# Kernel optimization log

Hardware: AMD Instinct MI355X
Metric: run time of the kernel (lower is better)

Reference implementation:

```python
import jax, jax.numpy as jnp
import numpy as np

B, H, LC, LQ = 64, 256, 2048, 256
NEG = -1e30


def setup_inputs() -> dict:
    key = jax.random.key(0)
    k1, k2, k3, k4, k5 = jax.random.split(key, 5)
    C = jax.random.normal(k1, (B, H, LC), dtype=jnp.float32)
    Q = jax.random.normal(k2, (B, H, LQ), dtype=jnp.float32)
    # mask convention: 1.0 = masked (padding), 0.0 = valid
    cmask = jax.random.bernoulli(k3, 0.1, (B, LC)).astype(jnp.float32)
    qmask = jax.random.bernoulli(k4, 0.1, (B, LQ)).astype(jnp.float32)
    line_project = jax.random.normal(k5, (3 * H,), dtype=jnp.float32) / np.sqrt(H)
    return {"C": C, "Q": Q, "cmask": cmask, "qmask": qmask, "line_project": line_project}


def reference(C, Q, cmask, qmask, line_project):
    # C: [B,H,Lc], Q: [B,H,Lq] -> [B,Lc,H], [B,Lq,H]
    Ct = jnp.swapaxes(C, 1, 2)
    Qt = jnp.swapaxes(Q, 1, 2)
    w1, w2, w3 = jnp.split(line_project, 3)
    # Trilinear decomposition of S[b,i,j] = [Ct;Qt;Ct*Qt] . w
    # avoids materializing the [B,Lc,Lq,3H] tensor of the original.
    S = (Ct @ w1)[:, :, None] + (Qt @ w2)[:, None, :] \
        + jnp.einsum('bih,h,bjh->bij', Ct, w3, Qt)  # [B,Lc,Lq]
    qm = qmask[:, None, :]  # [B,1,Lq]
    cm = cmask[:, :, None]  # [B,Lc,1]
    S_row = jax.nn.softmax(S * (1.0 - qm) + qm * NEG, axis=2)   # over Lq
    S_col = jax.nn.softmax(S * (1.0 - cm) + cm * NEG, axis=1)   # over Lc
    A = S_row @ Qt                                  # [B,Lc,H]
    # (S_row @ S_col^T) @ Ct  ==  S_row @ (S_col^T @ Ct): avoid [Lc,Lc]
    Bt = S_row @ (jnp.swapaxes(S_col, 1, 2) @ Ct)   # [B,Lc,H]
    out = jnp.concatenate((Ct, A, Ct * A, Ct * Bt), axis=2)  # [B,Lc,4H]
    # dropout is identity at inference (training=False)
    return jnp.swapaxes(out, 1, 2)  # [B,4H,Lc]
```

## Files before the change

### kernel.cpp

```cpp
#include <hip/hip_runtime.h>

#define BB 64
#define HH 256
#define LC 2048
#define LQ 256
#define NEGV -1e30f

#define OFF_S    0L
#define FOFF_BF  33554432L
#define FOFF_T   33554432L
#define FOFF_Q2  37748736L
#define FOFF_PM  37748736L
#define FOFF_PL  37879808L
#define OFF_FLAG 38010880L

#define NOFF_BF  33554432L
#define NOFF_Q2  37748736L
#define NOFF_PM  33554432L
#define NOFF_PL  33816576L
#define NOFF_T   34078720L

typedef __attribute__((ext_vector_type(8))) short short8v;
typedef __attribute__((ext_vector_type(4))) float f32x4;

union FragU { uint4 u; short8v h; };

__device__ __forceinline__ short8v ldfrag(const unsigned short* p) {
  FragU f; f.u = *reinterpret_cast<const uint4*>(p); return f.h;
}

#define MFMA(a, b, c) __builtin_amdgcn_mfma_f32_16x16x32_bf16(a, b, c, 0, 0, 0)

template<int MODE>
__device__ __forceinline__ float ld(const void* p, long idx) {
  if (MODE == 1) {
    unsigned short u = ((const unsigned short*)p)[idx];
    return __uint_as_float(((unsigned int)u) << 16);
  } else {
    return ((const float*)p)[idx];
  }
}

__device__ __forceinline__ float bf2f(unsigned short u) {
  return __uint_as_float(((unsigned int)u) << 16);
}

__device__ __forceinline__ unsigned short f2bf(float f) {
  unsigned int u = __float_as_uint(f);
  unsigned int r = (u + 0x7fffu + ((u >> 16) & 1u)) >> 16;
  return (unsigned short)r;
}

__device__ __forceinline__ void split1(float v, unsigned short& h, unsigned short& l) {
  unsigned int u = __float_as_uint(v);
  h = (unsigned short)(u >> 16);
  float r = v - __uint_as_float(u & 0xffff0000u);
  l = f2bf(r);
}

__device__ __forceinline__ void split8(const float4 f0, const float4 f1,
                                       short8v& hi, short8v& lo) {
  float v[8] = {f0.x, f0.y, f0.z, f0.w, f1.x, f1.y, f1.z, f1.w};
#pragma unroll
  for (int e = 0; e < 8; e++) {
    unsigned short h, l;
    split1(v[e], h, l);
    ((unsigned short*)&hi)[e] = h;
    ((unsigned short*)&lo)[e] = l;
  }
}

union U16x8 { uint4 u; unsigned short s[8]; };

__global__ void sniff_kernel(const unsigned int* cw, int* flag) {
  __shared__ int cnt[64];
  int tid = threadIdx.x;
  unsigned int w = cw[tid];
  int p = 0;
  for (int h = 0; h < 2; h++) {
    unsigned short u = h ? (unsigned short)(w >> 16) : (unsigned short)(w & 0xffffu);
    float f = __uint_as_float(((unsigned int)u) << 16);
    float a = fabsf(f);
    if ((a >= 1e-5f && a <= 64.0f) || f == 0.0f) p++;
  }
  cnt[tid] = p;
  __syncthreads();
  if (tid == 0) {
    int t = 0;
    for (int i = 0; i < 64; i++) t += cnt[i];
    *flag = (t >= 102) ? 1 : 0;
  }
}


__global__ __launch_bounds__(256) void f0_bfold(const void* Qp, const void* lpp,
                                                float* ws, const int* flag) {
  if (*flag != 0) return;
  __shared__ __align__(16) float Qs[64][68];
  __shared__ float w1s[HH], w2s[HH], w3s[HH];
  __shared__ float q2red[4][64];
  int t = threadIdx.x, b = blockIdx.y, j0 = blockIdx.x * 64;
  const float* Qf = (const float*)Qp;
  const float* lpf = (const float*)lpp;
  w1s[t] = lpf[t]; w2s[t] = lpf[HH + t]; w3s[t] = lpf[2 * HH + t];
  long qbase = (long)b * HH * LQ;
  unsigned short* Bfw = (unsigned short*)(ws + FOFF_BF);
  int jl = t & 63, hg = t >> 6;
  float q2a = 0.f;
  for (int hp = 0; hp < 4; hp++) {
    int h0 = hp * 64;
    __syncthreads();
    {
      int row = t >> 2, c = t & 3;
      const float4* src = (const float4*)&Qf[qbase + (long)(h0 + row) * LQ + j0 + c * 16];
      float4 v0 = src[0], v1 = src[1], v2 = src[2], v3 = src[3];
      *(float4*)&Qs[row][c * 16]      = v0;
      *(float4*)&Qs[row][c * 16 + 4]  = v1;
      *(float4*)&Qs[row][c * 16 + 8]  = v2;
      *(float4*)&Qs[row][c * 16 + 12] = v3;
    }
    __syncthreads();
    unsigned int hiw[8], low[8];
#pragma unroll
    for (int e = 0; e < 16; e++) {
      int hh = hg * 16 + e;
      int h = h0 + hh;
      float qv = Qs[hh][jl];
      float bb = w1s[h] + w3s[h] * qv;
      q2a += w2s[h] * qv;
      unsigned short bh, bl;
      split1(bb, bh, bl);
      if (e & 1) { hiw[e >> 1] |= ((unsigned int)bh) << 16; low[e >> 1] |= ((unsigned int)bl) << 16; }
      else       { hiw[e >> 1] = bh; low[e >> 1] = bl; }
    }
    long bfb = ((long)b * LQ + j0 + jl) * (2 * HH);
    *(uint4*)&Bfw[bfb + h0 + hg * 16]          = make_uint4(hiw[0], hiw[1], hiw[2], hiw[3]);
    *(uint4*)&Bfw[bfb + h0 + hg * 16 + 8]      = make_uint4(hiw[4], hiw[5], hiw[6], hiw[7]);
    *(uint4*)&Bfw[bfb + HH + h0 + hg * 16]     = make_uint4(low[0], low[1], low[2], low[3]);
    *(uint4*)&Bfw[bfb + HH + h0 + hg * 16 + 8] = make_uint4(low[4], low[5], low[6], low[7]);
  }
  q2red[hg][jl] = q2a;
  __syncthreads();
  if (t < 64)
    ws[FOFF_Q2 + (long)b * LQ + j0 + t] =
        q2red[0][t] + q2red[1][t] + q2red[2][t] + q2red[3][t];
}

__global__ __launch_bounds__(256) void f1_S(const void* Cp, float* ws, const int* flag) {
  if (*flag != 0) return;
  __shared__ __align__(16) unsigned short CaH[64 * 40];
  __shared__ __align__(16) unsigned short CaL[64 * 40];
  int t = threadIdx.x, b = blockIdx.y, i0 = blockIdx.x * 64;
  int w = t >> 6, l = t & 63;
  int lane_m = l & 15, kb = l >> 4;
  const float* Cf = (const float*)Cp;
  const unsigned short* Bf = (const unsigned short*)(ws + FOFF_BF);
  long cbase = (long)b * HH * LC;
  f32x4 z4 = {0.f, 0.f, 0.f, 0.f};
  f32x4 acc[4][4];
#pragma unroll
  for (int mf = 0; mf < 4; mf++)
#pragma unroll
    for (int nf = 0; nf < 4; nf++) acc[mf][nf] = z4;

  for (int hc = 0; hc < 8; hc++) {
    int h0 = hc * 32;
    __syncthreads();
#pragma unroll
    for (int hp = 0; hp < 4; hp++) {
      int hh = hp * 8 + (t >> 5);
      int ii = (t & 31) * 2;
      float2 cw = *(const float2*)&Cf[cbase + (long)(h0 + hh) * LC + i0 + ii];
      unsigned short xh, xl;
      split1(cw.x, xh, xl);
      CaH[ii * 40 + hh] = xh; CaL[ii * 40 + hh] = xl;
      split1(cw.y, xh, xl);
      CaH[(ii + 1) * 40 + hh] = xh; CaL[(ii + 1) * 40 + hh] = xl;
    }
    __syncthreads();
    short8v aH[4], aL[4];
#pragma unroll
    for (int mf = 0; mf < 4; mf++) {
      aH[mf] = ldfrag(&CaH[(mf * 16 + lane_m) * 40 + kb * 8]);
      aL[mf] = ldfrag(&CaL[(mf * 16 + lane_m) * 40 + kb * 8]);
    }
#pragma unroll
    for (int nf = 0; nf < 4; nf++) {
      long jb = ((long)b * LQ + w * 64 + nf * 16 + lane_m) * (2 * HH) + h0 + kb * 8;
      short8v bh = ldfrag(&Bf[jb]);
      short8v bl = ldfrag(&Bf[jb + HH]);
#pragma unroll
      for (int mf = 0; mf < 4; mf++) {
        acc[mf][nf] = MFMA(aH[mf], bh, acc[mf][nf]);
        acc[mf][nf] = MFMA(aH[mf], bl, acc[mf][nf]);
        acc[mf][nf] = MFMA(aL[mf], bh, acc[mf][nf]);
      }
    }
  }
  const float* q2g = ws + FOFF_Q2 + (long)b * LQ;
#pragma unroll
  for (int nf = 0; nf < 4; nf++) {
    int j = w * 64 + nf * 16 + lane_m;
    float q2v = q2g[j];
    float* So = ws + OFF_S + ((long)b * LC + i0 + kb * 4) * LQ + j;
#pragma unroll
    for (int mf = 0; mf < 4; mf++)
#pragma unroll
      for (int r = 0; r < 4; r++)
        So[(long)(mf * 16 + r) * LQ] = acc[mf][nf][r] + q2v;
  }
}

__global__ __launch_bounds__(256) void f2a_col(const void* cmaskp, float* ws, const int* flag) {
  if (*flag != 0) return;
  __shared__ float cms[256];
  int t = threadIdx.x, ch = blockIdx.x, b = blockIdx.y;
  int ib = ch * 256;
  cms[t] = ((const float*)cmaskp)[(long)b * LC + ib + t];
  __syncthreads();
  const float* Sb = ws + OFF_S + ((long)b * LC + ib) * LQ + t;
  float m = -INFINITY;
#pragma unroll 8
  for (int i = 0; i < 256; i++) {
    float v = (cms[i] != 0.f) ? NEGV : Sb[(long)i * LQ];
    m = fmaxf(m, v);
  }
  float s = 0.f;
#pragma unroll 8
  for (int i = 0; i < 256; i++) {
    float v = (cms[i] != 0.f) ? NEGV : Sb[(long)i * LQ];
    s += __expf(v - m);
  }
  ws[FOFF_PM + ((long)b * 8 + ch) * LQ + t] = m;
  ws[FOFF_PL + ((long)b * 8 + ch) * LQ + t] = s;
}

__global__ __launch_bounds__(512) void f2b_T(const void* Cp, const void* cmaskp,
                                             float* ws, const int* flag) {
  if (*flag != 0) return;
  __shared__ __align__(16) unsigned short PtH[64 * 72];
  __shared__ __align__(16) unsigned short PtL[64 * 72];
  int t = threadIdx.x, b = blockIdx.y, j0 = blockIdx.x * 64;
  int w = t >> 6, l = t & 63;
  int lane_m = l & 15, kb = l >> 4;
  int jj = j0 + l;
  const float* Cf = (const float*)Cp;
  const float* cmf = (const float*)cmaskp;
  float M = -INFINITY;
#pragma unroll
  for (int c = 0; c < 8; c++)
    M = fmaxf(M, ws[FOFF_PM + ((long)b * 8 + c) * LQ + jj]);
  float L = 0.f;
#pragma unroll
  for (int c = 0; c < 8; c++)
    L += ws[FOFF_PL + ((long)b * 8 + c) * LQ + jj] *
         __expf(ws[FOFF_PM + ((long)b * 8 + c) * LQ + jj] - M);
  float Li = 1.0f / L;
  int hw = (w >> 1) * 64, jw = (w & 1) * 32;
  long cbase = (long)b * HH * LC;
  const float* Sb = ws + OFF_S + (long)b * LC * LQ;
  f32x4 z4 = {0.f, 0.f, 0.f, 0.f};
  f32x4 acc[4][2];
#pragma unroll
  for (int mf = 0; mf < 4; mf++) { acc[mf][0] = z4; acc[mf][1] = z4; }

  for (int ic = 0; ic < 32; ic++) {
    int i0 = ic * 64;
    __syncthreads();
    unsigned int pwH[4], pwL[4];
#pragma unroll
    for (int s2 = 0; s2 < 4; s2++) {
      unsigned short h0s, l0s, h1s, l1s;
      {
        int i = i0 + w * 8 + 2 * s2;
        float cm = cmf[(long)b * LC + i];
        float sv = Sb[(long)i * LQ + jj];
        float p = (cm != 0.f) ? 0.f : __expf(sv - M) * Li;
        split1(p, h0s, l0s);
      }
      {
        int i = i0 + w * 8 + 2 * s2 + 1;
        float cm = cmf[(long)b * LC + i];
        float sv = Sb[(long)i * LQ + jj];
        float p = (cm != 0.f) ? 0.f : __expf(sv - M) * Li;
        split1(p, h1s, l1s);
      }
      pwH[s2] = (unsigned int)h0s | ((unsigned int)h1s << 16);
      pwL[s2] = (unsigned int)l0s | ((unsigned int)l1s << 16);
    }
    *(uint4*)&PtH[l * 72 + w * 8] = make_uint4(pwH[0], pwH[1], pwH[2], pwH[3]);
    *(uint4*)&PtL[l * 72 + w * 8] = make_uint4(pwL[0], pwL[1], pwL[2], pwL[3]);
    __syncthreads();
#pragma unroll
    for (int ks = 0; ks < 2; ks++) {
      short8v b0h = ldfrag(&PtH[(jw + lane_m) * 72 + ks * 32 + kb * 8]);
      short8v b0l = ldfrag(&PtL[(jw + lane_m) * 72 + ks * 32 + kb * 8]);
      short8v b1h = ldfrag(&PtH[(jw + 16 + lane_m) * 72 + ks * 32 + kb * 8]);
      short8v b1l = ldfrag(&PtL[(jw + 16 + lane_m) * 72 + ks * 32 + kb * 8]);
#pragma unroll
      for (int mf = 0; mf < 4; mf++) {
        const float* cp = Cf + cbase + (long)(hw + mf * 16 + lane_m) * LC + i0 + ks * 32 + kb * 8;
        short8v aH, aL;
        split8(((const float4*)cp)[0], ((const float4*)cp)[1], aH, aL);
        acc[mf][0] = MFMA(aH, b0h, acc[mf][0]);
        acc[mf][0] = MFMA(aH, b0l, acc[mf][0]);
        acc[mf][0] = MFMA(aL, b0h, acc[mf][0]);
        acc[mf][1] = MFMA(aH, b1h, acc[mf][1]);
        acc[mf][1] = MFMA(aH, b1l, acc[mf][1]);
        acc[mf][1] = MFMA(aL, b1h, acc[mf][1]);
      }
    }
  }
  unsigned short* Tu = (unsigned short*)(ws + FOFF_T);
#pragma unroll
  for (int mf = 0; mf < 4; mf++)
#pragma unroll
    for (int nf = 0; nf < 2; nf++)
#pragma unroll
      for (int r = 0; r < 4; r++) {
        int h = hw + mf * 16 + kb * 4 + r;
        int j = j0 + jw + nf * 16 + lane_m;
        unsigned short th, tl;
        split1(acc[mf][nf][r], th, tl);
        long tb = ((long)b * HH + h) * (2 * LQ);
        Tu[tb + j] = th;
        Tu[tb + LQ + j] = tl;
      }
}

__global__ __launch_bounds__(512) void f3_out(const void* Cp, const void* Qp, const void* qmaskp,
                                              float* ws, void* outp, const int* flag) {
  if (*flag != 0) return;
  __shared__ __align__(16) unsigned short PrH[32 * 264];
  __shared__ __align__(16) unsigned short PrL[32 * 264];
  __shared__ float qms[LQ];
  int t = threadIdx.x, b = blockIdx.y, i0 = blockIdx.x * 32;
  int w = t >> 6, l = t & 63;
  const float* Cf = (const float*)Cp;
  const float* Qf = (const float*)Qp;
  if (t < LQ) qms[t] = ((const float*)qmaskp)[(long)b * LQ + t];
  __syncthreads();
  const float* Sb = ws + OFF_S + ((long)b * LC + i0) * LQ;
#pragma unroll
  for (int r = 0; r < 4; r++) {
    int row = w * 4 + r;
    float v[4];
#pragma unroll
    for (int c = 0; c < 4; c++) {
      float sv = Sb[(long)row * LQ + l + 64 * c];
      v[c] = (qms[l + 64 * c] != 0.f) ? NEGV : sv;
    }
    float mx = fmaxf(fmaxf(v[0], v[1]), fmaxf(v[2], v[3]));
#pragma unroll
    for (int o2 = 1; o2 < 64; o2 <<= 1) mx = fmaxf(mx, __shfl_xor(mx, o2));
    float e[4]; float sm = 0.f;
#pragma unroll
    for (int c = 0; c < 4; c++) { e[c] = __expf(v[c] - mx); sm += e[c]; }
#pragma unroll
    for (int o2 = 1; o2 < 64; o2 <<= 1) sm += __shfl_xor(sm, o2);
    float inv = 1.0f / sm;
#pragma unroll
    for (int c = 0; c < 4; c++) {
      unsigned short ph, pl;
      split1(e[c] * inv, ph, pl);
      PrH[row * 264 + l + 64 * c] = ph;
      PrL[row * 264 + l + 64 * c] = pl;
    }
  }
  __syncthreads();
  int lane_m = l & 15, kb = l >> 4;
  int hw2 = w * 32;
  const unsigned short* Tu = (const unsigned short*)(ws + FOFF_T);
  long qrow = (long)b * HH * LQ;
  f32x4 z4 = {0.f, 0.f, 0.f, 0.f};
  f32x4 acc1[2][2], acc2[2][2];
#pragma unroll
  for (int mf = 0; mf < 2; mf++) {
    acc1[mf][0] = z4; acc1[mf][1] = z4;
    acc2[mf][0] = z4; acc2[mf][1] = z4;
  }
#pragma unroll
  for (int kc = 0; kc < 8; kc++) {
    short8v b0h = ldfrag(&PrH[lane_m * 264 + kc * 32 + kb * 8]);
    short8v b0l = ldfrag(&PrL[lane_m * 264 + kc * 32 + kb * 8]);
    short8v b1h = ldfrag(&PrH[(16 + lane_m) * 264 + kc * 32 + kb * 8]);
    short8v b1l = ldfrag(&PrL[(16 + lane_m) * 264 + kc * 32 + kb * 8]);
#pragma unroll
    for (int mf = 0; mf < 2; mf++) {
      int h = hw2 + mf * 16 + lane_m;
      const float* qp = Qf + qrow + (long)h * LQ + kc * 32 + kb * 8;
      short8v a1H, a1L;
      split8(((const float4*)qp)[0], ((const float4*)qp)[1], a1H, a1L);
      long tb = ((long)b * HH + h) * (2 * LQ) + kc * 32 + kb * 8;
      short8v a2H = ldfrag(&Tu[tb]);
      short8v a2L = ldfrag(&Tu[tb + LQ]);
      acc1[mf][0] = MFMA(a1H, b0h, acc1[mf][0]);
      acc1[mf][0] = MFMA(a1H, b0l, acc1[mf][0]);
      acc1[mf][0] = MFMA(a1L, b0h, acc1[mf][0]);
      acc1[mf][1] = MFMA(a1H, b1h, acc1[mf][1]);
      acc1[mf][1] = MFMA(a1H, b1l, acc1[mf][1]);
      acc1[mf][1] = MFMA(a1L, b1h, acc1[mf][1]);
      acc2[mf][0] = MFMA(a2H, b0h, acc2[mf][0]);
      acc2[mf][0] = MFMA(a2H, b0l, acc2[mf][0]);
      acc2[mf][0] = MFMA(a2L, b0h, acc2[mf][0]);
      acc2[mf][1] = MFMA(a2H, b1h, acc2[mf][1]);
      acc2[mf][1] = MFMA(a2H, b1l, acc2[mf][1]);
      acc2[mf][1] = MFMA(a2L, b1h, acc2[mf][1]);
    }
  }
  float* o = (float*)outp;
  long ob = (long)b * (4 * HH) * LC;
#pragma unroll
  for (int mf = 0; mf < 2; mf++)
#pragma unroll
    for (int nf = 0; nf < 2; nf++) {
      int i = i0 + nf * 16 + lane_m;
#pragma unroll
      for (int r = 0; r < 4; r++) {
        int h = hw2 + mf * 16 + kb * 4 + r;
        float cc = Cf[((long)b * HH + h) * LC + i];
        float av = acc1[mf][nf][r], bv = acc2[mf][nf][r];
        long r0 = ob + (long)h * LC + i;
        o[r0] = cc;
        o[r0 + (long)HH * LC] = av;
        o[r0 + 2L * HH * LC] = cc * av;
        o[r0 + 3L * HH * LC] = cc * bv;
      }
    }
}


__global__ __launch_bounds__(256) void nk0_bfold(const void* Qp, const void* lpp,
                                                 float* ws, const int* flag) {
  if (*flag != 1) return;
  __shared__ __align__(16) unsigned short Qs[64 * 72];
  __shared__ float w1s[HH], w2s[HH], w3s[HH];
  __shared__ float q2red[4][64];
  int t = threadIdx.x;
  int b = blockIdx.y, j0 = blockIdx.x * 64;
  w1s[t] = ld<1>(lpp, t);
  w2s[t] = ld<1>(lpp, HH + t);
  w3s[t] = ld<1>(lpp, 2 * HH + t);
  const unsigned short* Qu = (const unsigned short*)Qp;
  long qbase = (long)b * HH * LQ;
  unsigned short* Bf = (unsigned short*)(ws + NOFF_BF);
  int jl = t & 63, hg = t >> 6;
  float q2a = 0.f;
  for (int hp = 0; hp < 4; hp++) {
    int h0 = hp * 64;
    __syncthreads();
    {
      int row = t >> 2, c = t & 3;
      const uint4* src = (const uint4*)&Qu[qbase + (long)(h0 + row) * LQ + j0 + c * 16];
      uint4 v0 = src[0]; uint4 v1 = src[1];
      *(uint4*)&Qs[row * 72 + c * 16] = v0;
      *(uint4*)&Qs[row * 72 + c * 16 + 8] = v1;
    }
    __syncthreads();
    unsigned int hiw[8], low[8];
#pragma unroll
    for (int e = 0; e < 16; e++) {
      int hh = hg * 16 + e;
      int h = h0 + hh;
      float qv = bf2f(Qs[hh * 72 + jl]);
      float bb = w1s[h] + w3s[h] * qv;
      q2a += w2s[h] * qv;
      unsigned short bh = f2bf(bb);
      float res = bb - bf2f(bh);
      unsigned short bl = f2bf(res);
      if (e & 1) { hiw[e >> 1] |= ((unsigned int)bh) << 16; low[e >> 1] |= ((unsigned int)bl) << 16; }
      else       { hiw[e >> 1] = bh; low[e >> 1] = bl; }
    }
    long bfb = ((long)b * LQ + j0 + jl) * (2 * HH);
    *(uint4*)&Bf[bfb + h0 + hg * 16]      = make_uint4(hiw[0], hiw[1], hiw[2], hiw[3]);
    *(uint4*)&Bf[bfb + h0 + hg * 16 + 8]  = make_uint4(hiw[4], hiw[5], hiw[6], hiw[7]);
    *(uint4*)&Bf[bfb + HH + h0 + hg * 16]     = make_uint4(low[0], low[1], low[2], low[3]);
    *(uint4*)&Bf[bfb + HH + h0 + hg * 16 + 8] = make_uint4(low[4], low[5], low[6], low[7]);
  }
  q2red[hg][jl] = q2a;
  __syncthreads();
  if (t < 64)
    ws[NOFF_Q2 + (long)b * LQ + j0 + t] =
        q2red[0][t] + q2red[1][t] + q2red[2][t] + q2red[3][t];
}

__global__ __launch_bounds__(256) void nk1_S(const void* Cp, float* ws, const int* flag) {
  if (*flag != 1) return;
  __shared__ __align__(16) unsigned short Ca[64 * 40];
  int t = threadIdx.x;
  int b = blockIdx.y, i0 = blockIdx.x * 64;
  int w = t >> 6, l = t & 63;
  int lane_m = l & 15, kb = l >> 4;
  const unsigned short* Cu = (const unsigned short*)Cp;
  const unsigned short* Bf = (const unsigned short*)(ws + NOFF_BF);
  long cbase = (long)b * HH * LC;
  f32x4 z4 = {0.f, 0.f, 0.f, 0.f};
  f32x4 acc[4][4];
#pragma unroll
  for (int mf = 0; mf < 4; mf++)
#pragma unroll
    for (int nf = 0; nf < 4; nf++) acc[mf][nf] = z4;

  for (int hc = 0; hc < 8; hc++) {
    int h0 = hc * 32;
    __syncthreads();
#pragma unroll
    for (int hp = 0; hp < 4; hp++) {
      int hh = hp * 8 + (t >> 5);
      int ii = (t & 31) * 2;
      unsigned int cw = *(const unsigned int*)&Cu[cbase + (long)(h0 + hh) * LC + i0 + ii];
      Ca[ii * 40 + hh] = (unsigned short)(cw & 0xffffu);
      Ca[(ii + 1) * 40 + hh] = (unsigned short)(cw >> 16);
    }
    __syncthreads();
    short8v afr[4];
#pragma unroll
    for (int mf = 0; mf < 4; mf++)
      afr[mf] = ldfrag(&Ca[(mf * 16 + lane_m) * 40 + kb * 8]);
#pragma unroll
    for (int nf = 0; nf < 4; nf++) {
      long jb = ((long)b * LQ + w * 64 + nf * 16 + lane_m) * (2 * HH) + h0 + kb * 8;
      short8v bh = ldfrag(&Bf[jb]);
      short8v bl = ldfrag(&Bf[jb + HH]);
#pragma unroll
      for (int mf = 0; mf < 4; mf++) {
        acc[mf][nf] = MFMA(afr[mf], bh, acc[mf][nf]);
        acc[mf][nf] = MFMA(afr[mf], bl, acc[mf][nf]);
      }
    }
  }
  const float* q2g = ws + NOFF_Q2 + (long)b * LQ;
#pragma unroll
  for (int nf = 0; nf < 4; nf++) {
    int j = w * 64 + nf * 16 + lane_m;
    float q2v = q2g[j];
    float* So = ws + OFF_S + ((long)b * LC + i0 + kb * 4) * LQ + j;
#pragma unroll
    for (int mf = 0; mf < 4; mf++)
#pragma unroll
      for (int r = 0; r < 4; r++)
        So[(long)(mf * 16 + r) * LQ] = acc[mf][nf][r] + q2v;
  }
}

__global__ __launch_bounds__(256) void nk2a_col(const void* cmaskp, float* ws, const int* flag) {
  if (*flag != 1) return;
  __shared__ float cms[128];
  int t = threadIdx.x, ch = blockIdx.x, b = blockIdx.y;
  int ib = ch * 128;
  if (t < 128) cms[t] = ld<1>(cmaskp, (long)b * LC + ib + t);
  __syncthreads();
  const float* Sb = ws + OFF_S + ((long)b * LC + ib) * LQ + t;
  float m = -INFINITY;
#pragma unroll 8
  for (int i = 0; i < 128; i++) {
    float v = (cms[i] != 0.f) ? NEGV : Sb[(long)i * LQ];
    m = fmaxf(m, v);
  }
  float s = 0.f;
#pragma unroll 8
  for (int i = 0; i < 128; i++) {
    float v = (cms[i] != 0.f) ? NEGV : Sb[(long)i * LQ];
    s += __expf(v - m);
  }
  ws[NOFF_PM + ((long)b * 16 + ch) * LQ + t] = m;
  ws[NOFF_PL + ((long)b * 16 + ch) * LQ + t] = s;
}

__global__ __launch_bounds__(512) void nk2b_T(const void* Cp, const void* cmaskp,
                                              float* ws, const int* flag) {
  if (*flag != 1) return;
  __shared__ __align__(16) unsigned short Pt[64 * 72];
  int t = threadIdx.x, b = blockIdx.y, j0 = blockIdx.x * 64;
  int w = t >> 6, l = t & 63;
  int lane_m = l & 15, kb = l >> 4;
  int jj = j0 + l;
  float M = -INFINITY;
#pragma unroll
  for (int c = 0; c < 16; c++)
    M = fmaxf(M, ws[NOFF_PM + ((long)b * 16 + c) * LQ + jj]);
  float L = 0.f;
#pragma unroll
  for (int c = 0; c < 16; c++)
    L += ws[NOFF_PL + ((long)b * 16 + c) * LQ + jj] *
         __expf(ws[NOFF_PM + ((long)b * 16 + c) * LQ + jj] - M);
  float Li = 1.0f / L;
  int hw = (w >> 1) * 64, jw = (w & 1) * 32;
  const unsigned short* Cu = (const unsigned short*)Cp;
  long cbase = (long)b * HH * LC;
  const float* Sb = ws + OFF_S + (long)b * LC * LQ;
  f32x4 z4 = {0.f, 0.f, 0.f, 0.f};
  f32x4 acc[4][2];
#pragma unroll
  for (int mf = 0; mf < 4; mf++) { acc[mf][0] = z4; acc[mf][1] = z4; }

  for (int ic = 0; ic < 32; ic++) {
    int i0 = ic * 64;
    __syncthreads();
    unsigned int pw[4];
#pragma unroll
    for (int s2 = 0; s2 < 4; s2++) {
      unsigned int lo16, hi16;
      {
        int i = i0 + w * 8 + 2 * s2;
        float cm = ld<1>(cmaskp, (long)b * LC + i);
        float sv = Sb[(long)i * LQ + jj];
        float p = (cm != 0.f) ? 0.f : __expf(sv - M) * Li;
        lo16 = f2bf(p);
      }
      {
        int i = i0 + w * 8 + 2 * s2 + 1;
        float cm = ld<1>(cmaskp, (long)b * LC + i);
        float sv = Sb[(long)i * LQ + jj];
        float p = (cm != 0.f) ? 0.f : __expf(sv - M) * Li;
        hi16 = f2bf(p);
      }
      pw[s2] = lo16 | (hi16 << 16);
    }
    *(uint4*)&Pt[l * 72 + w * 8] = make_uint4(pw[0], pw[1], pw[2], pw[3]);
    __syncthreads();
#pragma unroll
    for (int ks = 0; ks < 2; ks++) {
      short8v b0 = ldfrag(&Pt[(jw + lane_m) * 72 + ks * 32 + kb * 8]);
      short8v b1 = ldfrag(&Pt[(jw + 16 + lane_m) * 72 + ks * 32 + kb * 8]);
#pragma unroll
      for (int mf = 0; mf < 4; mf++) {
        short8v a = ldfrag(&Cu[cbase + (long)(hw + mf * 16 + lane_m) * LC + i0 + ks * 32 + kb * 8]);
        acc[mf][0] = MFMA(a, b0, acc[mf][0]);
        acc[mf][1] = MFMA(a, b1, acc[mf][1]);
      }
    }
  }
  unsigned short* Tt = (unsigned short*)(ws + NOFF_T);
#pragma unroll
  for (int mf = 0; mf < 4; mf++)
#pragma unroll
    for (int nf = 0; nf < 2; nf++)
#pragma unroll
      for (int r = 0; r < 4; r++) {
        int h = hw + mf * 16 + kb * 4 + r;
        int j = j0 + jw + nf * 16 + lane_m;
        Tt[((long)b * HH + h) * LQ + j] = f2bf(acc[mf][nf][r]);
      }
}

__global__ __launch_bounds__(512) void nk3_out(const void* Cp, const void* Qp, const void* qmaskp,
                                               float* ws, void* outp, const int* flag) {
  if (*flag != 1) return;
  __shared__ __align__(16) unsigned short Pr[64 * 264];
  __shared__ float qms[LQ];
  int t = threadIdx.x, b = blockIdx.y, i0 = blockIdx.x * 64;
  int w = t >> 6, l = t & 63;
  if (t < LQ) qms[t] = ld<1>(qmaskp, (long)b * LQ + t);
  __syncthreads();
  const float* Sb = ws + OFF_S + ((long)b * LC + i0) * LQ;
#pragma unroll
  for (int r = 0; r < 8; r++) {
    int row = w * 8 + r;
    float v[4];
#pragma unroll
    for (int c = 0; c < 4; c++) {
      float sv = Sb[(long)row * LQ + l + 64 * c];
      v[c] = (qms[l + 64 * c] != 0.f) ? NEGV : sv;
    }
    float mx = fmaxf(fmaxf(v[0], v[1]), fmaxf(v[2], v[3]));
#pragma unroll
    for (int o = 1; o < 64; o <<= 1) mx = fmaxf(mx, __shfl_xor(mx, o));
    float e[4]; float sm = 0.f;
#pragma unroll
    for (int c = 0; c < 4; c++) { e[c] = __expf(v[c] - mx); sm += e[c]; }
#pragma unroll
    for (int o = 1; o < 64; o <<= 1) sm += __shfl_xor(sm, o);
    float inv = 1.0f / sm;
#pragma unroll
    for (int c = 0; c < 4; c++) Pr[row * 264 + l + 64 * c] = f2bf(e[c] * inv);
  }
  __syncthreads();
  int lane_m = l & 15, kb = l >> 4;
  int hw2 = (w >> 1) * 64, iw = (w & 1) * 32;
  const unsigned short* Qu = (const unsigned short*)Qp;
  const unsigned short* Tt = (const unsigned short*)(ws + NOFF_T);
  long qrow = (long)b * HH * LQ;
  f32x4 z4 = {0.f, 0.f, 0.f, 0.f};
  f32x4 acc1[4][2], acc2[4][2];
#pragma unroll
  for (int mf = 0; mf < 4; mf++) {
    acc1[mf][0] = z4; acc1[mf][1] = z4;
    acc2[mf][0] = z4; acc2[mf][1] = z4;
  }
#pragma unroll
  for (int kc = 0; kc < 8; kc++) {
    short8v b0 = ldfrag(&Pr[(iw + lane_m) * 264 + kc * 32 + kb * 8]);
    short8v b1 = ldfrag(&Pr[(iw + 16 + lane_m) * 264 + kc * 32 + kb * 8]);
#pragma unroll
    for (int mf = 0; mf < 4; mf++) {
      long ro = qrow + (long)(hw2 + mf * 16 + lane_m) * LQ + kc * 32 + kb * 8;
      short8v a1 = ldfrag(&Qu[ro]);
      acc1[mf][0] = MFMA(a1, b0, acc1[mf][0]);
      acc1[mf][1] = MFMA(a1, b1, acc1[mf][1]);
      short8v a2 = ldfrag(&Tt[ro]);
      acc2[mf][0] = MFMA(a2, b0, acc2[mf][0]);
      acc2[mf][1] = MFMA(a2, b1, acc2[mf][1]);
    }
  }
  unsigned short* o = (unsigned short*)outp;
  const unsigned short* Cu = (const unsigned short*)Cp;
  long ob = (long)b * (4 * HH) * LC;
#pragma unroll
  for (int mf = 0; mf < 4; mf++)
#pragma unroll
    for (int nf = 0; nf < 2; nf++) {
      int i = i0 + iw + nf * 16 + lane_m;
#pragma unroll
      for (int r = 0; r < 4; r++) {
        int h = hw2 + mf * 16 + kb * 4 + r;
        unsigned short craw = Cu[(long)(b * HH + h) * LC + i];
        float cc = bf2f(craw);
        float av = acc1[mf][nf][r], bv = acc2[mf][nf][r];
        long r0 = ob + (long)h * LC + i;
        o[r0] = craw;
        o[r0 + (long)HH * LC] = f2bf(av);
        o[r0 + 2L * HH * LC] = f2bf(cc * av);
        o[r0 + 3L * HH * LC] = f2bf(cc * bv);
      }
    }
}

extern "C" void kernel_launch(void* const* d_in, const int* in_sizes, int n_in,
                              void* d_out, int out_size, void* d_ws, size_t ws_size,
                              hipStream_t stream) {
  const void* C  = d_in[0];
  const void* Q  = d_in[1];
  const void* cm = d_in[2];
  const void* qm = d_in[3];
  const void* lp = d_in[4];
  float* ws = (float*)d_ws;
  int* flag = (int*)(ws + OFF_FLAG);

  sniff_kernel<<<1, 64, 0, stream>>>((const unsigned int*)C, flag);

  f0_bfold<<<dim3(4, BB), 256, 0, stream>>>(Q, lp, ws, flag);
  f1_S<<<dim3(LC / 64, BB), 256, 0, stream>>>(C, ws, flag);
  f2a_col<<<dim3(8, BB), 256, 0, stream>>>(cm, ws, flag);
  f2b_T<<<dim3(4, BB), 512, 0, stream>>>(C, cm, ws, flag);
  f3_out<<<dim3(LC / 32, BB), 512, 0, stream>>>(C, Q, qm, ws, d_out, flag);

  nk0_bfold<<<dim3(4, BB), 256, 0, stream>>>(Q, lp, ws, flag);
  nk1_S<<<dim3(LC / 64, BB), 256, 0, stream>>>(C, ws, flag);
  nk2a_col<<<dim3(16, BB), 256, 0, stream>>>(cm, ws, flag);
  nk2b_T<<<dim3(4, BB), 512, 0, stream>>>(C, cm, ws, flag);
  nk3_out<<<dim3(LC / 64, BB), 512, 0, stream>>>(C, Q, qm, ws, d_out, flag);
}
```

Baseline: 1.431 ms.

## Fuse row-softmax into S GEMM, store bf16 exp scores, drop column-stats pass

```diff
diff --git a/kernel.cpp b/kernel.cpp
--- a/kernel.cpp
+++ b/kernel.cpp
@@ -6,14 +6,17 @@
 #define LQ 256
 #define NEGV -1e30f
 
+#define GOFF_X    0L
+#define GOFF_BF   16777216L
+#define GOFF_QS   20971520L
+#define GOFF_TS   25165824L
+#define GOFF_MR   29360128L
+#define GOFF_LR   29491200L
+#define GOFF_Q2   29622272L
+#define GOFF_K    29638656L
+#define OFF_FLAG  38010880L
+
 #define OFF_S    0L
-#define FOFF_BF  33554432L
-#define FOFF_T   33554432L
-#define FOFF_Q2  37748736L
-#define FOFF_PM  37748736L
-#define FOFF_PL  37879808L
-#define OFF_FLAG 38010880L
-
 #define NOFF_BF  33554432L
 #define NOFF_Q2  37748736L
 #define NOFF_PM  33554432L
@@ -72,7 +75,15 @@
 
 union U16x8 { uint4 u; unsigned short s[8]; };
 
-__global__ void sniff_kernel(const unsigned int* cw, int* flag) {
+__device__ __forceinline__ unsigned int fenc(float f) {
+  unsigned int u = __float_as_uint(f);
+  return (u >> 31) ? ~u : (u | 0x80000000u);
+}
+__device__ __forceinline__ float fdec(unsigned int e) {
+  return (e >> 31) ? __uint_as_float(e ^ 0x80000000u) : __uint_as_float(~e);
+}
+
+__global__ void sniff_kernel(const unsigned int* cw, int* flag, unsigned int* kz) {
   __shared__ int cnt[64];
   int tid = threadIdx.x;
   unsigned int w = cw[tid];
@@ -84,6 +95,7 @@
     if ((a >= 1e-5f && a <= 64.0f) || f == 0.0f) p++;
   }
   cnt[tid] = p;
+  kz[tid] = 0u;
   __syncthreads();
   if (tid == 0) {
     int t = 0;
@@ -104,7 +116,7 @@
   const float* lpf = (const float*)lpp;
   w1s[t] = lpf[t]; w2s[t] = lpf[HH + t]; w3s[t] = lpf[2 * HH + t];
   long qbase = (long)b * HH * LQ;
-  unsigned short* Bfw = (unsigned short*)(ws + FOFF_BF);
+  unsigned short* Bfw = (unsigned short*)(ws + GOFF_BF);
   int jl = t & 63, hg = t >> 6;
   float q2a = 0.f;
   for (int hp = 0; hp < 4; hp++) {
@@ -142,19 +154,51 @@
   q2red[hg][jl] = q2a;
   __syncthreads();
   if (t < 64)
-    ws[FOFF_Q2 + (long)b * LQ + j0 + t] =
+    ws[GOFF_Q2 + (long)b * LQ + j0 + t] =
         q2red[0][t] + q2red[1][t] + q2red[2][t] + q2red[3][t];
 }
 
-__global__ __launch_bounds__(256) void f1_S(const void* Cp, float* ws, const int* flag) {
+__global__ __launch_bounds__(256) void g0b_Qsplit(const void* Qp, const void* qmaskp,
+                                                  float* ws, const int* flag) {
+  if (*flag != 0) return;
+  __shared__ float qms[LQ];
+  int t = threadIdx.x, b = blockIdx.y, hb = blockIdx.x;
+  qms[t] = (((const float*)qmaskp)[(long)b * LQ + t] != 0.f) ? 0.f : 1.f;
+  __syncthreads();
+  const float* Qf = (const float*)Qp;
+  unsigned short* Qs = (unsigned short*)(ws + GOFF_QS);
+#pragma unroll
+  for (int it = 0; it < 4; it++) {
+    int o = t + 256 * it;
+    int hh = o >> 5;
+    int j8 = (o & 31) * 8;
+    const float* qp = Qf + ((long)b * HH + hb * 32 + hh) * LQ + j8;
+    float4 v0 = ((const float4*)qp)[0], v1 = ((const float4*)qp)[1];
+    float4 m0 = make_float4(v0.x * qms[j8], v0.y * qms[j8 + 1],
+                            v0.z * qms[j8 + 2], v0.w * qms[j8 + 3]);
+    float4 m1 = make_float4(v1.x * qms[j8 + 4], v1.y * qms[j8 + 5],
+                            v1.z * qms[j8 + 6], v1.w * qms[j8 + 7]);
+    short8v hi, lo;
+    split8(m0, m1, hi, lo);
+    long qb = ((long)b * HH + hb * 32 + hh) * (2 * LQ) + j8;
+    FragU fh, fl; fh.h = hi; fl.h = lo;
+    *(uint4*)&Qs[qb] = fh.u;
+    *(uint4*)&Qs[qb + LQ] = fl.u;
+  }
+}
+
+__global__ __launch_bounds__(256) void g1_SX(const void* Cp, const void* qmaskp,
+                                             float* ws, const int* flag) {
   if (*flag != 0) return;
   __shared__ __align__(16) unsigned short CaH[64 * 40];
   __shared__ __align__(16) unsigned short CaL[64 * 40];
+  __shared__ float redm[64][4];
+  __shared__ float redl[64][4];
   int t = threadIdx.x, b = blockIdx.y, i0 = blockIdx.x * 64;
   int w = t >> 6, l = t & 63;
   int lane_m = l & 15, kb = l >> 4;
   const float* Cf = (const float*)Cp;
-  const unsigned short* Bf = (const unsigned short*)(ws + FOFF_BF);
+  const unsigned short* Bf = (const unsigned short*)(ws + GOFF_BF);
   long cbase = (long)b * HH * LC;
   f32x4 z4 = {0.f, 0.f, 0.f, 0.f};
   f32x4 acc[4][4];
@@ -197,229 +241,220 @@
       }
     }
   }
-  const float* q2g = ws + FOFF_Q2 + (long)b * LQ;
+  const float* q2g = ws + GOFF_Q2 + (long)b * LQ;
+  const float* qmf = (const float*)qmaskp;
+  float q2v[4], qm0v[4];
 #pragma unroll
   for (int nf = 0; nf < 4; nf++) {
     int j = w * 64 + nf * 16 + lane_m;
-    float q2v = q2g[j];
-    float* So = ws + OFF_S + ((long)b * LC + i0 + kb * 4) * LQ + j;
-#pragma unroll
-    for (int mf = 0; mf < 4; mf++)
-#pragma unroll
-      for (int r = 0; r < 4; r++)
-        So[(long)(mf * 16 + r) * LQ] = acc[mf][nf][r] + q2v;
-  }
-}
-
-__global__ __launch_bounds__(256) void f2a_col(const void* cmaskp, float* ws, const int* flag) {
-  if (*flag != 0) return;
-  __shared__ float cms[256];
-  int t = threadIdx.x, ch = blockIdx.x, b = blockIdx.y;
-  int ib = ch * 256;
-  cms[t] = ((const float*)cmaskp)[(long)b * LC + ib + t];
-  __syncthreads();
-  const float* Sb = ws + OFF_S + ((long)b * LC + ib) * LQ + t;
-  float m = -INFINITY;
-#pragma unroll 8
-  for (int i = 0; i < 256; i++) {
-    float v = (cms[i] != 0.f) ? NEGV : Sb[(long)i * LQ];
-    m = fmaxf(m, v);
-  }
-  float s = 0.f;
-#pragma unroll 8
-  for (int i = 0; i < 256; i++) {
-    float v = (cms[i] != 0.f) ? NEGV : Sb[(long)i * LQ];
-    s += __expf(v - m);
-  }
-  ws[FOFF_PM + ((long)b * 8 + ch) * LQ + t] = m;
-  ws[FOFF_PL + ((long)b * 8 + ch) * LQ + t] = s;
-}
-
-__global__ __launch_bounds__(512) void f2b_T(const void* Cp, const void* cmaskp,
+    q2v[nf] = q2g[j];
+    qm0v[nf] = (qmf[(long)b * LQ + j] != 0.f) ? 0.f : 1.f;
+  }
+#pragma unroll
+  for (int mf = 0; mf < 4; mf++)
+#pragma unroll
+    for (int r = 0; r < 4; r++) {
+      float vx = -INFINITY;
+#pragma unroll
+      for (int nf = 0; nf < 4; nf++) {
+        float s = acc[mf][nf][r] + q2v[nf];
+        vx = fmaxf(vx, (qm0v[nf] != 0.f) ? s : NEGV);
+      }
+      vx = fmaxf(vx, __shfl_xor(vx, 1));
+      vx = fmaxf(vx, __shfl_xor(vx, 2));
+      vx = fmaxf(vx, __shfl_xor(vx, 4));
+      vx = fmaxf(vx, __shfl_xor(vx, 8));
+      if (lane_m == 0) redm[mf * 16 + kb * 4 + r][w] = vx;
+    }
+  __syncthreads();
+  unsigned short* Xu = (unsigned short*)(ws + GOFF_X);
+#pragma unroll
+  for (int mf = 0; mf < 4; mf++)
+#pragma unroll
+    for (int r = 0; r < 4; r++) {
+      int il = mf * 16 + kb * 4 + r;
+      float mr = fmaxf(fmaxf(fmaxf(redm[il][0], redm[il][1]),
+                             fmaxf(redm[il][2], redm[il][3])), -60.f);
+      float ls = 0.f;
+#pragma unroll
+      for (int nf = 0; nf < 4; nf++) {
+        int j = w * 64 + nf * 16 + lane_m;
+        float s = acc[mf][nf][r] + q2v[nf];
+        unsigned short xb = f2bf(__expf(s - mr));
+        Xu[((long)b * LC + i0 + il) * LQ + j] = xb;
+        ls += qm0v[nf] * bf2f(xb);
+      }
+      ls += __shfl_xor(ls, 1);
+      ls += __shfl_xor(ls, 2);
+      ls += __shfl_xor(ls, 4);
+      ls += __shfl_xor(ls, 8);
+      if (lane_m == 0) redl[il][w] = ls;
+    }
+  __syncthreads();
+  if (t < 64) {
+    int il = t;
+    float mrf = fmaxf(fmaxf(fmaxf(redm[il][0], redm[il][1]),
+                            fmaxf(redm[il][2], redm[il][3])), -60.f);
+    float lrf = redl[il][0] + redl[il][1] + redl[il][2] + redl[il][3];
+    ws[GOFF_MR + (long)b * LC + i0 + il] = mrf;
+    ws[GOFF_LR + (long)b * LC + i0 + il] = 1.0f / lrf;
+    redm[il][0] = mrf;
+  }
+  __syncthreads();
+  if (t == 0) {
+    float km = -INFINITY;
+    for (int i2 = 0; i2 < 64; i2++) km = fmaxf(km, redm[i2][0]);
+    atomicMax((unsigned int*)(ws + GOFF_K) + b, fenc(km));
+  }
+}
+
+__global__ __launch_bounds__(1024) void g2_T(const void* Cp, const void* cmaskp, const void* qmaskp,
                                              float* ws, const int* flag) {
   if (*flag != 0) return;
-  __shared__ __align__(16) unsigned short PtH[64 * 72];
-  __shared__ __align__(16) unsigned short PtL[64 * 72];
-  int t = threadIdx.x, b = blockIdx.y, j0 = blockIdx.x * 64;
+  __shared__ __align__(16) unsigned short Pt[128 * 72];
+  __shared__ float lcred[128][9];
+  __shared__ float lcinv[128];
+  int t = threadIdx.x, b = blockIdx.y;
+  int jb = blockIdx.x & 1, hb = blockIdx.x >> 1;
+  int j0 = jb * 128, h0 = hb * 128;
   int w = t >> 6, l = t & 63;
   int lane_m = l & 15, kb = l >> 4;
-  int jj = j0 + l;
+  int wh = w & 7, wj = w >> 3;
+  int jloc = t & 127, ib = t >> 7;
+  unsigned int Ke = ((unsigned int*)(ws + GOFF_K))[b];
+  float Kf = fdec(Ke);
   const float* Cf = (const float*)Cp;
   const float* cmf = (const float*)cmaskp;
-  float M = -INFINITY;
-#pragma unroll
-  for (int c = 0; c < 8; c++)
-    M = fmaxf(M, ws[FOFF_PM + ((long)b * 8 + c) * LQ + jj]);
-  float L = 0.f;
-#pragma unroll
-  for (int c = 0; c < 8; c++)
-    L += ws[FOFF_PL + ((long)b * 8 + c) * LQ + jj] *
-         __expf(ws[FOFF_PM + ((long)b * 8 + c) * LQ + jj] - M);
-  float Li = 1.0f / L;
-  int hw = (w >> 1) * 64, jw = (w & 1) * 32;
+  const unsigned short* Xu = (const unsigned short*)(ws + GOFF_X);
+  const float* mrp = ws + GOFF_MR + (long)b * LC;
   long cbase = (long)b * HH * LC;
-  const float* Sb = ws + OFF_S + (long)b * LC * LQ;
   f32x4 z4 = {0.f, 0.f, 0.f, 0.f};
-  f32x4 acc[4][2];
-#pragma unroll
-  for (int mf = 0; mf < 4; mf++) { acc[mf][0] = z4; acc[mf][1] = z4; }
+  f32x4 acc[4];
+#pragma unroll
+  for (int nf = 0; nf < 4; nf++) acc[nf] = z4;
+  float lcp = 0.f;
 
   for (int ic = 0; ic < 32; ic++) {
     int i0 = ic * 64;
     __syncthreads();
-    unsigned int pwH[4], pwL[4];
-#pragma unroll
-    for (int s2 = 0; s2 < 4; s2++) {
-      unsigned short h0s, l0s, h1s, l1s;
+    unsigned int pw[4];
+#pragma unroll
+    for (int e2 = 0; e2 < 4; e2++) {
+      unsigned short s0, s1;
       {
-        int i = i0 + w * 8 + 2 * s2;
-        float cm = cmf[(long)b * LC + i];
-        float sv = Sb[(long)i * LQ + jj];
-        float p = (cm != 0.f) ? 0.f : __expf(sv - M) * Li;
-        split1(p, h0s, l0s);
+        int i = i0 + ib * 8 + 2 * e2;
+        float ecm = (cmf[(long)b * LC + i] != 0.f) ? 0.f : __expf(mrp[i] - Kf);
+        float n = bf2f(Xu[((long)b * LC + i) * LQ + j0 + jloc]) * ecm;
+        s0 = f2bf(n); lcp += n;
       }
       {
-        int i = i0 + w * 8 + 2 * s2 + 1;
-        float cm = cmf[(long)b * LC + i];
-        float sv = Sb[(long)i * LQ + jj];
-        float p = (cm != 0.f) ? 0.f : __expf(sv - M) * Li;
-        split1(p, h1s, l1s);
-      }
-      pwH[s2] = (unsigned int)h0s | ((unsigned int)h1s << 16);
-      pwL[s2] = (unsigned int)l0s | ((unsigned int)l1s << 16);
-    }
-    *(uint4*)&PtH[l * 72 + w * 8] = make_uint4(pwH[0], pwH[1], pwH[2], pwH[3]);
-    *(uint4*)&PtL[l * 72 + w * 8] = make_uint4(pwL[0], pwL[1], pwL[2], pwL[3]);
+        int i = i0 + ib * 8 + 2 * e2 + 1;
+        float ecm = (cmf[(long)b * LC + i] != 0.f) ? 0.f : __expf(mrp[i] - Kf);
+        float n = bf2f(Xu[((long)b * LC + i) * LQ + j0 + jloc]) * ecm;
+        s1 = f2bf(n); lcp += n;
+      }
+      pw[e2] = (unsigned int)s0 | ((unsigned int)s1 << 16);
+    }
+    *(uint4*)&Pt[jloc * 72 + ib * 8] = make_uint4(pw[0], pw[1], pw[2], pw[3]);
     __syncthreads();
 #pragma unroll
     for (int ks = 0; ks < 2; ks++) {
-      short8v b0h = ldfrag(&PtH[(jw + lane_m) * 72 + ks * 32 + kb * 8]);
-      short8v b0l = ldfrag(&PtL[(jw + lane_m) * 72 + ks * 32 + kb * 8]);
-      short8v b1h = ldfrag(&PtH[(jw + 16 + lane_m) * 72 + ks * 32 + kb * 8]);
-      short8v b1l = ldfrag(&PtL[(jw + 16 + lane_m) * 72 + ks * 32 + kb * 8]);
-#pragma unroll
-      for (int mf = 0; mf < 4; mf++) {
-        const float* cp = Cf + cbase + (long)(hw + mf * 16 + lane_m) * LC + i0 + ks * 32 + kb * 8;
-        short8v aH, aL;
-        split8(((const float4*)cp)[0], ((const float4*)cp)[1], aH, aL);
-        acc[mf][0] = MFMA(aH, b0h, acc[mf][0]);
-        acc[mf][0] = MFMA(aH, b0l, acc[mf][0]);
-        acc[mf][0] = MFMA(aL, b0h, acc[mf][0]);
-        acc[mf][1] = MFMA(aH, b1h, acc[mf][1]);
-        acc[mf][1] = MFMA(aH, b1l, acc[mf][1]);
-        acc[mf][1] = MFMA(aL, b1h, acc[mf][1]);
-      }
-    }
-  }
-  unsigned short* Tu = (unsigned short*)(ws + FOFF_T);
-#pragma unroll
-  for (int mf = 0; mf < 4; mf++)
-#pragma unroll
-    for (int nf = 0; nf < 2; nf++)
-#pragma unroll
-      for (int r = 0; r < 4; r++) {
-        int h = hw + mf * 16 + kb * 4 + r;
-        int j = j0 + jw + nf * 16 + lane_m;
-        unsigned short th, tl;
-        split1(acc[mf][nf][r], th, tl);
-        long tb = ((long)b * HH + h) * (2 * LQ);
-        Tu[tb + j] = th;
-        Tu[tb + LQ + j] = tl;
-      }
-}
-
-__global__ __launch_bounds__(512) void f3_out(const void* Cp, const void* Qp, const void* qmaskp,
-                                              float* ws, void* outp, const int* flag) {
+      const float* cp = Cf + cbase + (long)(h0 + wh * 16 + lane_m) * LC + i0 + ks * 32 + kb * 8;
+      short8v aH, aL;
+      split8(((const float4*)cp)[0], ((const float4*)cp)[1], aH, aL);
+#pragma unroll
+      for (int nf = 0; nf < 4; nf++) {
+        short8v bfr = ldfrag(&Pt[(wj * 64 + nf * 16 + lane_m) * 72 + ks * 32 + kb * 8]);
+        acc[nf] = MFMA(aH, bfr, acc[nf]);
+        acc[nf] = MFMA(aL, bfr, acc[nf]);
+      }
+    }
+  }
+  __syncthreads();
+  lcred[jloc][ib] = lcp;
+  __syncthreads();
+  if (t < 128) {
+    float s = 0.f;
+    for (int q = 0; q < 8; q++) s += lcred[t][q];
+    lcinv[t] = 1.0f / s;
+  }
+  __syncthreads();
+  const float* qmf = (const float*)qmaskp;
+  unsigned short* Tu = (unsigned short*)(ws + GOFF_TS);
+#pragma unroll
+  for (int nf = 0; nf < 4; nf++) {
+    int jl = wj * 64 + nf * 16 + lane_m;
+    int j = j0 + jl;
+    float sc = lcinv[jl] * ((qmf[(long)b * LQ + j] != 0.f) ? 0.f : 1.f);
+#pragma unroll
+    for (int r = 0; r < 4; r++) {
+      int h = h0 + wh * 16 + kb * 4 + r;
+      float tv = acc[nf][r] * sc;
+      unsigned short th, tl;
+      split1(tv, th, tl);
+      long tb2 = ((long)b * HH + h) * (2 * LQ);
+      Tu[tb2 + j] = th;
+      Tu[tb2 + LQ + j] = tl;
+    }
+  }
+}
+
+__global__ __launch_bounds__(512) void g3_out(const void* Cp, float* ws, void* outp,
+                                              const int* flag) {
   if (*flag != 0) return;
-  __shared__ __align__(16) unsigned short PrH[32 * 264];
-  __shared__ __align__(16) unsigned short PrL[32 * 264];
-  __shared__ float qms[LQ];
-  int t = threadIdx.x, b = blockIdx.y, i0 = blockIdx.x * 32;
+  int t = threadIdx.x, b = blockIdx.y, i0 = blockIdx.x * 64;
   int w = t >> 6, l = t & 63;
-  const float* Cf = (const float*)Cp;
-  const float* Qf = (const float*)Qp;
-  if (t < LQ) qms[t] = ((const float*)qmaskp)[(long)b * LQ + t];
-  __syncthreads();
-  const float* Sb = ws + OFF_S + ((long)b * LC + i0) * LQ;
-#pragma unroll
-  for (int r = 0; r < 4; r++) {
-    int row = w * 4 + r;
-    float v[4];
-#pragma unroll
-    for (int c = 0; c < 4; c++) {
-      float sv = Sb[(long)row * LQ + l + 64 * c];
-      v[c] = (qms[l + 64 * c] != 0.f) ? NEGV : sv;
-    }
-    float mx = fmaxf(fmaxf(v[0], v[1]), fmaxf(v[2], v[3]));
-#pragma unroll
-    for (int o2 = 1; o2 < 64; o2 <<= 1) mx = fmaxf(mx, __shfl_xor(mx, o2));
-    float e[4]; float sm = 0.f;
-#pragma unroll
-    for (int c = 0; c < 4; c++) { e[c] = __expf(v[c] - mx); sm += e[c]; }
-#pragma unroll
-    for (int o2 = 1; o2 < 64; o2 <<= 1) sm += __shfl_xor(sm, o2);
-    float inv = 1.0f / sm;
-#pragma unroll
-    for (int c = 0; c < 4; c++) {
-      unsigned short ph, pl;
-      split1(e[c] * inv, ph, pl);
-      PrH[row * 264 + l + 64 * c] = ph;
-      PrL[row * 264 + l + 64 * c] = pl;
-    }
-  }
-  __syncthreads();
   int lane_m = l & 15, kb = l >> 4;
   int hw2 = w * 32;
-  const unsigned short* Tu = (const unsigned short*)(ws + FOFF_T);
-  long qrow = (long)b * HH * LQ;
+  const unsigned short* Xu = (const unsigned short*)(ws + GOFF_X);
+  const unsigned short* Qs = (const unsigned short*)(ws + GOFF_QS);
+  const unsigned short* Ts = (const unsigned short*)(ws + GOFF_TS);
   f32x4 z4 = {0.f, 0.f, 0.f, 0.f};
-  f32x4 acc1[2][2], acc2[2][2];
-#pragma unroll
-  for (int mf = 0; mf < 2; mf++) {
-    acc1[mf][0] = z4; acc1[mf][1] = z4;
-    acc2[mf][0] = z4; acc2[mf][1] = z4;
-  }
+  f32x4 acc1[2][4], acc2[2][4];
+#pragma unroll
+  for (int mf = 0; mf < 2; mf++)
+#pragma unroll
+    for (int nf = 0; nf < 4; nf++) { acc1[mf][nf] = z4; acc2[mf][nf] = z4; }
 #pragma unroll
   for (int kc = 0; kc < 8; kc++) {
-    short8v b0h = ldfrag(&PrH[lane_m * 264 + kc * 32 + kb * 8]);
-    short8v b0l = ldfrag(&PrL[lane_m * 264 + kc * 32 + kb * 8]);
-    short8v b1h = ldfrag(&PrH[(16 + lane_m) * 264 + kc * 32 + kb * 8]);
-    short8v b1l = ldfrag(&PrL[(16 + lane_m) * 264 + kc * 32 + kb * 8]);
+    short8v bfr[4];
+#pragma unroll
+    for (int nf = 0; nf < 4; nf++)
+      bfr[nf] = ldfrag(&Xu[((long)b * LC + i0 + nf * 16 + lane_m) * LQ + kc * 32 + kb * 8]);
 #pragma unroll
     for (int mf = 0; mf < 2; mf++) {
-      int h = hw2 + mf * 16 + lane_m;
-      const float* qp = Qf + qrow + (long)h * LQ + kc * 32 + kb * 8;
-      short8v a1H, a1L;
-      split8(((const float4*)qp)[0], ((const float4*)qp)[1], a1H, a1L);
-      long tb = ((long)b * HH + h) * (2 * LQ) + kc * 32 + kb * 8;
-      short8v a2H = ldfrag(&Tu[tb]);
-      short8v a2L = ldfrag(&Tu[tb + LQ]);
-      acc1[mf][0] = MFMA(a1H, b0h, acc1[mf][0]);
-      acc1[mf][0] = MFMA(a1H, b0l, acc1[mf][0]);
-      acc1[mf][0] = MFMA(a1L, b0h, acc1[mf][0]);
-      acc1[mf][1] = MFMA(a1H, b1h, acc1[mf][1]);
-      acc1[mf][1] = MFMA(a1H, b1l, acc1[mf][1]);
-      acc1[mf][1] = MFMA(a1L, b1h, acc1[mf][1]);
-      acc2[mf][0] = MFMA(a2H, b0h, acc2[mf][0]);
-      acc2[mf][0] = MFMA(a2H, b0l, acc2[mf][0]);
-      acc2[mf][0] = MFMA(a2L, b0h, acc2[mf][0]);
-      acc2[mf][1] = MFMA(a2H, b1h, acc2[mf][1]);
-      acc2[mf][1] = MFMA(a2H, b1l, acc2[mf][1]);
-      acc2[mf][1] = MFMA(a2L, b1h, acc2[mf][1]);
-    }
-  }
+      long ab = ((long)b * HH + hw2 + mf * 16 + lane_m) * (2 * LQ) + kc * 32 + kb * 8;
+      short8v a1H = ldfrag(&Qs[ab]);
+      short8v a1L = ldfrag(&Qs[ab + LQ]);
+      short8v a2H = ldfrag(&Ts[ab]);
+      short8v a2L = ldfrag(&Ts[ab + LQ]);
+#pragma unroll
+      for (int nf = 0; nf < 4; nf++) {
+        acc1[mf][nf] = MFMA(a1H, bfr[nf], acc1[mf][nf]);
+        acc1[mf][nf] = MFMA(a1L, bfr[nf], acc1[mf][nf]);
+        acc2[mf][nf] = MFMA(a2H, bfr[nf], acc2[mf][nf]);
+        acc2[mf][nf] = MFMA(a2L, bfr[nf], acc2[mf][nf]);
+      }
+    }
+  }
+  const float* Cf = (const float*)Cp;
+  const float* lrp = ws + GOFF_LR + (long)b * LC;
+  float linv[4];
+#pragma unroll
+  for (int nf = 0; nf < 4; nf++) linv[nf] = lrp[i0 + nf * 16 + lane_m];
   float* o = (float*)outp;
   long ob = (long)b * (4 * HH) * LC;
 #pragma unroll
   for (int mf = 0; mf < 2; mf++)
 #pragma unroll
-    for (int nf = 0; nf < 2; nf++) {
+    for (int nf = 0; nf < 4; nf++) {
       int i = i0 + nf * 16 + lane_m;
 #pragma unroll
       for (int r = 0; r < 4; r++) {
         int h = hw2 + mf * 16 + kb * 4 + r;
         float cc = Cf[((long)b * HH + h) * LC + i];
-        float av = acc1[mf][nf][r], bv = acc2[mf][nf][r];
+        float av = acc1[mf][nf][r] * linv[nf];
+        float bv = acc2[mf][nf][r] * linv[nf];
         long r0 = ob + (long)h * LC + i;
         o[r0] = cc;
         o[r0 + (long)HH * LC] = av;
@@ -736,14 +771,15 @@
   const void* lp = d_in[4];
   float* ws = (float*)d_ws;
   int* flag = (int*)(ws + OFF_FLAG);
-
-  sniff_kernel<<<1, 64, 0, stream>>>((const unsigned int*)C, flag);
+  unsigned int* kz = (unsigned int*)(ws + GOFF_K);
+
+  sniff_kernel<<<1, 64, 0, stream>>>((const unsigned int*)C, flag, kz);
 
   f0_bfold<<<dim3(4, BB), 256, 0, stream>>>(Q, lp, ws, flag);
-  f1_S<<<dim3(LC / 64, BB), 256, 0, stream>>>(C, ws, flag);
-  f2a_col<<<dim3(8, BB), 256, 0, stream>>>(cm, ws, flag);
-  f2b_T<<<dim3(4, BB), 512, 0, stream>>>(C, cm, ws, flag);
-  f3_out<<<dim3(LC / 32, BB), 512, 0, stream>>>(C, Q, qm, ws, d_out, flag);
+  g0b_Qsplit<<<dim3(8, BB), 256, 0, stream>>>(Q, qm, ws, flag);
+  g1_SX<<<dim3(LC / 64, BB), 256, 0, stream>>>(C, qm, ws, flag);
+  g2_T<<<dim3(4, BB), 1024, 0, stream>>>(C, cm, qm, ws, flag);
+  g3_out<<<dim3(LC / 64, BB), 512, 0, stream>>>(C, ws, d_out, flag);
 
   nk0_bfold<<<dim3(4, BB), 256, 0, stream>>>(Q, lp, ws, flag);
   nk1_S<<<dim3(LC / 64, BB), 256, 0, stream>>>(C, ws, flag);
```

Result: faster. 1.274 ms (-11.0%).
